# Optimization experiments

Hardware: AMD Instinct MI355X
Metric: run time of the kernel (lower is better)

## Reference

```python
import jax, jax.numpy as jnp
import numpy as np
import math

N_HEADS = 16
DIM = 1024
D_HEAD = DIM // N_HEADS
BS, QLEN = 2, 2048


def setup_inputs() -> dict:
    key = jax.random.key(0)
    ks = jax.random.split(key, 10)
    s = 0.02
    return {
        "input": jax.random.normal(ks[0], (BS, QLEN, DIM), dtype=jnp.float32),
        "mask": jnp.ones((BS, QLEN), dtype=jnp.int32),
        "q_w": jax.random.normal(ks[1], (DIM, DIM), dtype=jnp.float32) * s,
        "q_b": jax.random.normal(ks[2], (DIM,), dtype=jnp.float32) * s,
        "k_w": jax.random.normal(ks[3], (DIM, DIM), dtype=jnp.float32) * s,
        "k_b": jax.random.normal(ks[4], (DIM,), dtype=jnp.float32) * s,
        "v_w": jax.random.normal(ks[5], (DIM, DIM), dtype=jnp.float32) * s,
        "v_b": jax.random.normal(ks[6], (DIM,), dtype=jnp.float32) * s,
        "o_w": jax.random.normal(ks[7], (DIM, DIM), dtype=jnp.float32) * s,
        "o_b": jax.random.normal(ks[8], (DIM,), dtype=jnp.float32) * s,
    }


def _shape(x, bs):
    # (bs, len, dim) -> (bs, heads, len, d_head)
    return x.reshape(bs, -1, N_HEADS, D_HEAD).transpose(0, 2, 1, 3)


def reference(input, mask, q_w, q_b, k_w, k_b, v_w, v_b, o_w, o_b):
    bs, qlen, dim = input.shape
    # projections (torch Linear: x @ W^T + b)
    q = _shape(input @ q_w.T + q_b, bs)
    k = _shape(input @ k_w.T + k_b, bs)
    v = _shape(input @ v_w.T + v_b, bs)
    q = q / math.sqrt(D_HEAD)
    # scores: (bs, heads, qlen, klen)
    scores = jnp.einsum("bhqd,bhkd->bhqk", q, k)
    pad = (mask == 0)[:, None, None, :]  # (bs,1,1,klen)
    scores = jnp.where(pad, -jnp.inf, scores)
    weights = jax.nn.softmax(scores.astype(jnp.float32), axis=-1).astype(scores.dtype)
    # dropout p=0.0 (eval) -> identity
    context = jnp.einsum("bhqk,bhkd->bhqd", weights, v)
    context = context.transpose(0, 2, 1, 3).reshape(bs, qlen, dim)
    return context @ o_w.T + o_b
```

## Files before the change

### kernel.cpp

```cpp
#include <hip/hip_runtime.h>


#define BS    2
#define QLEN  2048
#define DIM   1024
#define NH    16
#define DH    64
#define MTOK  (BS * QLEN)

#define QSCALE 0.18033688011112042f

typedef __attribute__((ext_vector_type(8))) short short8;
typedef __attribute__((ext_vector_type(4))) float float4_t;
typedef __attribute__((ext_vector_type(4))) int   int4_t;

__device__ __forceinline__ ushort f2bf(float f) {
    unsigned u = __float_as_uint(f);
    return (ushort)((u + 0x7fffu + ((u >> 16) & 1u)) >> 16);
}
__device__ __forceinline__ short8 pack8(float4 a0, float4 a1) {
    short8 r;
    r[0] = (short)f2bf(a0.x); r[1] = (short)f2bf(a0.y);
    r[2] = (short)f2bf(a0.z); r[3] = (short)f2bf(a0.w);
    r[4] = (short)f2bf(a1.x); r[5] = (short)f2bf(a1.y);
    r[6] = (short)f2bf(a1.z); r[7] = (short)f2bf(a1.w);
    return r;
}

__device__ __forceinline__ void glds16(const void* g, void* l) {
    __builtin_amdgcn_global_load_lds(
        (const __attribute__((address_space(1))) unsigned int*)g,
        (__attribute__((address_space(3))) unsigned int*)l, 16, 0, 0);
}

__global__ __launch_bounds__(256) void conv_all(
    const float* __restrict__ x,  const float* __restrict__ qw,
    const float* __restrict__ kw, const float* __restrict__ vw,
    const float* __restrict__ ow,
    ushort* __restrict__ Xbf, ushort* __restrict__ Wbf)
{
    const int blk = blockIdx.x;
    const float* s; ushort* d; size_t base;
    if (blk < 4096)      { s = x;  d = Xbf;             base = (size_t)blk * 1024; }
    else if (blk < 5120) { s = qw; d = Wbf;             base = (size_t)(blk - 4096) * 1024; }
    else if (blk < 6144) { s = kw; d = Wbf + 1048576;   base = (size_t)(blk - 5120) * 1024; }
    else if (blk < 7168) { s = vw; d = Wbf + 2097152;   base = (size_t)(blk - 6144) * 1024; }
    else                 { s = ow; d = Wbf + 3145728;   base = (size_t)(blk - 7168) * 1024; }
    const size_t i = base + threadIdx.x * 4;
    float4 v = *(const float4*)(s + i);
    ushort4 o;
    o.x = f2bf(v.x); o.y = f2bf(v.y); o.z = f2bf(v.z); o.w = f2bf(v.w);
    *(ushort4*)(d + i) = o;
}

__global__ __launch_bounds__(256) void transpose_v(
    const ushort* __restrict__ Vrow, ushort* __restrict__ Vt)
{
    __shared__ ushort T[64][72];
    const int tid  = threadIdx.x;
    const int tile = blockIdx.x;
    const int bh   = blockIdx.y;
    const int b = bh >> 4, h = bh & 15;

    #pragma unroll
    for (int rep = 0; rep < 2; ++rep) {
        int ch = tid + rep * 256;
        int tok = ch >> 3, seg = ch & 7;
        uint4 v = *(const uint4*)(Vrow + (size_t)(b * QLEN + tile * 64 + tok) * DIM
                                        + h * DH + seg * 8);
        *(uint4*)&T[tok][seg * 8] = v;
    }
    __syncthreads();
    #pragma unroll
    for (int rep = 0; rep < 2; ++rep) {
        int ch = tid + rep * 256;
        int dim = ch >> 3, tseg = ch & 7;
        ushort t0 = T[tseg * 8 + 0][dim], t1 = T[tseg * 8 + 1][dim];
        ushort t2 = T[tseg * 8 + 2][dim], t3 = T[tseg * 8 + 3][dim];
        ushort t4 = T[tseg * 8 + 4][dim], t5 = T[tseg * 8 + 5][dim];
        ushort t6 = T[tseg * 8 + 6][dim], t7 = T[tseg * 8 + 7][dim];
        uint4 o;
        o.x = (unsigned)t0 | ((unsigned)t1 << 16);
        o.y = (unsigned)t2 | ((unsigned)t3 << 16);
        o.z = (unsigned)t4 | ((unsigned)t5 << 16);
        o.w = (unsigned)t6 | ((unsigned)t7 << 16);
        *(uint4*)(Vt + (size_t)bh * DH * QLEN + (size_t)dim * QLEN
                      + tile * 64 + tseg * 8) = o;
    }
}

__global__ __launch_bounds__(512, 2) void gemm_qkv(
    const ushort* __restrict__ A, const ushort* __restrict__ Bw,
    const float* __restrict__ bias0, const float* __restrict__ bias1,
    const float* __restrict__ bias2,
    ushort* __restrict__ outQ, ushort* __restrict__ outK, ushort* __restrict__ outVt)
{
    __shared__ ushort As[2][256 * 64];
    __shared__ ushort Bs[2][192 * 64];

    const int tid  = threadIdx.x;
    const int w    = tid >> 6;
    const int lane = tid & 63;
    const int r15  = lane & 15;
    const int quad = lane >> 4;
    const int wm   = w >> 2;
    const int wn   = w & 3;
    const int xg   = r15 & 7;

    const int xcd = blockIdx.x & 7;
    const int lid = blockIdx.x >> 3;
    const int brow = (xcd & 3) * 4 + (lid & 3);
    const int bcol = (xcd >> 2) * 8 + (lid >> 2);
    const int K = DIM;

    float4_t acc[8][3];
    #pragma unroll
    for (int i = 0; i < 8; ++i)
        #pragma unroll
        for (int j = 0; j < 3; ++j)
            acc[i][j] = (float4_t){0.f, 0.f, 0.f, 0.f};

    const ushort* gaS[4];
    const ushort* gbS[3];
    #pragma unroll
    for (int rep = 0; rep < 4; ++rep) {
        const int c   = rep * 512 + tid;
        const int row = c >> 3;
        const int g   = (c & 7) ^ (row & 7);
        gaS[rep] = A + (size_t)(brow * 256 + row) * K + g * 8;
    }
    #pragma unroll
    for (int rep = 0; rep < 3; ++rep) {
        const int c   = rep * 512 + tid;
        const int row = c >> 3;
        const int g   = (c & 7) ^ (row & 7);
        gbS[rep] = Bw + (size_t)(bcol * 192 + row) * K + g * 8;
    }

    short8 afr[2][4];
    short8 bfr[2][3];

#define QBAR() do { asm volatile("" ::: "memory");                            \
                    __builtin_amdgcn_s_barrier();                             \
                    asm volatile("" ::: "memory"); } while (0)
#define QVM0() asm volatile("s_waitcnt vmcnt(0)" ::: "memory")

#define STAGE_T(BUFI, KOFF) do {                                              \
    _Pragma("unroll")                                                         \
    for (int rep = 0; rep < 4; ++rep)                                         \
        glds16(gaS[rep] + (KOFF), &As[BUFI][(rep * 512 + tid) * 8]);          \
    _Pragma("unroll")                                                         \
    for (int rep = 0; rep < 3; ++rep)                                         \
        glds16(gbS[rep] + (KOFF), &Bs[BUFI][(rep * 512 + tid) * 8]);          \
} while (0)

#define PH_B(BUFI) do {                                                       \
    _Pragma("unroll")                                                         \
    for (int hh = 0; hh < 2; ++hh) {                                          \
        const int ph = ((hh * 4 + quad) ^ xg) * 8;                            \
        _Pragma("unroll")                                                     \
        for (int ns = 0; ns < 3; ++ns)                                        \
            bfr[hh][ns] = *(const short8*)&Bs[BUFI][(wn * 48 + ns * 16 + r15) * 64 + ph]; \
    }                                                                         \
} while (0)

#define PH_A(BUFI, MH) do {                                                   \
    const int arow0 = wm * 128 + (MH) * 64;                                   \
    _Pragma("unroll")                                                         \
    for (int hh = 0; hh < 2; ++hh) {                                          \
        const int ph = ((hh * 4 + quad) ^ xg) * 8;                            \
        _Pragma("unroll")                                                     \
        for (int ms = 0; ms < 4; ++ms)                                        \
            afr[hh][ms] = *(const short8*)&As[BUFI][(arow0 + ms * 16 + r15) * 64 + ph]; \
    }                                                                         \
} while (0)

#define MFMA_MH(MH) do {                                                      \
    __builtin_amdgcn_s_setprio(1);                                            \
    _Pragma("unroll")                                                         \
    for (int hh = 0; hh < 2; ++hh)                                            \
        _Pragma("unroll")                                                     \
        for (int ms = 0; ms < 4; ++ms)                                        \
            _Pragma("unroll")                                                 \
            for (int ns = 0; ns < 3; ++ns)                                    \
                acc[(MH) * 4 + ms][ns] =                                      \
                    __builtin_amdgcn_mfma_f32_16x16x32_bf16(                  \
                        afr[hh][ms], bfr[hh][ns], acc[(MH) * 4 + ms][ns], 0, 0, 0); \
    __builtin_amdgcn_s_setprio(0);                                            \
} while (0)

#define QITER(KB, LAST) do {                                                  \
    STAGE_T(1, (KB) + 64);                                                    \
    PH_B(0); PH_A(0, 0); MFMA_MH(0);                 QBAR();                  \
    PH_A(0, 1); MFMA_MH(1); QVM0();                  QBAR();                  \
    if (!(LAST)) STAGE_T(0, (KB) + 128);                                      \
    PH_B(1); PH_A(1, 0); MFMA_MH(0);                 QBAR();                  \
    PH_A(1, 1); MFMA_MH(1); if (!(LAST)) { QVM0(); } QBAR();                  \
} while (0)

    STAGE_T(0, 0);
    QVM0();
    QBAR();

    for (int i = 0; i < 7; ++i)
        QITER(i * 128, 0);
    QITER(896, 1);

#undef QITER
#undef MFMA_MH
#undef PH_A
#undef PH_B
#undef STAGE_T
#undef QVM0
#undef QBAR

    #pragma unroll
    for (int msg = 0; msg < 8; ++msg) {
        const int rowg = brow * 256 + wm * 128 + msg * 16 + quad * 4;
        #pragma unroll
        for (int nsg = 0; nsg < 3; ++nsg) {
            const int colg = bcol * 192 + wn * 48 + nsg * 16 + r15;
            if (colg < 1024) {
                const float bb = bias0[colg];
                #pragma unroll
                for (int r = 0; r < 4; ++r)
                    outQ[(size_t)(rowg + r) * 1024 + colg] =
                        f2bf((acc[msg][nsg][r] + bb) * QSCALE);
            } else if (colg < 2048) {
                const float bb = bias1[colg - 1024];
                #pragma unroll
                for (int r = 0; r < 4; ++r)
                    outK[(size_t)(rowg + r) * 1024 + (colg - 1024)] =
                        f2bf(acc[msg][nsg][r] + bb);
            } else {
                const int vcol = colg - 2048;
                const int hh2 = vcol >> 6, dd = vcol & 63;
                const float bb = bias2[vcol];
                const int bidx = rowg >> 11;
                const int tloc = rowg & 2047;
                ushort4 o4;
                o4.x = f2bf(acc[msg][nsg][0] + bb);
                o4.y = f2bf(acc[msg][nsg][1] + bb);
                o4.z = f2bf(acc[msg][nsg][2] + bb);
                o4.w = f2bf(acc[msg][nsg][3] + bb);
                *(ushort4*)&outVt[((size_t)(bidx * 16 + hh2) * 64 + dd) * QLEN + tloc] = o4;
            }
        }
    }
}

__global__ __launch_bounds__(256) void gemm_o(
    const ushort* __restrict__ A, const ushort* __restrict__ Bw,
    const float* __restrict__ bias, float* __restrict__ Out)
{
    __shared__ ushort As[2][128 * 64];
    __shared__ ushort Bs[2][64 * 64];
    const int tid  = threadIdx.x;
    const int w    = tid >> 6;
    const int lane = tid & 63;
    const int r15  = lane & 15;
    const int quad = lane >> 4;
    const int xcd = blockIdx.x & 7;
    const int lid = blockIdx.x >> 3;
    const int brow = (xcd & 3) * 8 + (lid & 7);
    const int bcol = (xcd >> 2) * 8 + (lid >> 3);
    const int wrow = w * 32;
    const int K = DIM;

    float4_t acc[2][4];
    #pragma unroll
    for (int i = 0; i < 2; ++i)
        #pragma unroll
        for (int j = 0; j < 4; ++j)
            acc[i][j] = (float4_t){0.f, 0.f, 0.f, 0.f};

    int chA[4];  const ushort* gaS[4];
    #pragma unroll
    for (int rep = 0; rep < 4; ++rep) {
        const int ch  = w * 256 + rep * 64 + lane;
        const int row = ch >> 3;
        const int g   = (ch & 7) ^ (row & 7);
        chA[rep] = ch;
        gaS[rep] = A + (size_t)(brow * 128 + row) * K + g * 8;
    }
    int chB[2];  const ushort* gbS[2];
    #pragma unroll
    for (int rep = 0; rep < 2; ++rep) {
        const int ch  = w * 128 + rep * 64 + lane;
        const int row = ch >> 3;
        const int g   = (ch & 7) ^ (row & 7);
        chB[rep] = ch;
        gbS[rep] = Bw + (size_t)(bcol * 64 + row) * K + g * 8;
    }
    const int xg = r15 & 7;

    #pragma unroll
    for (int rep = 0; rep < 4; ++rep)
        glds16(gaS[rep], &As[0][chA[rep] * 8]);
    #pragma unroll
    for (int rep = 0; rep < 2; ++rep)
        glds16(gbS[rep], &Bs[0][chB[rep] * 8]);
    __syncthreads();

    int p = 0;
    for (int k0 = 0; k0 < K; k0 += 64) {
        if (k0 + 64 < K) {
            #pragma unroll
            for (int rep = 0; rep < 4; ++rep)
                glds16(gaS[rep] + k0 + 64, &As[p ^ 1][chA[rep] * 8]);
            #pragma unroll
            for (int rep = 0; rep < 2; ++rep)
                glds16(gbS[rep] + k0 + 64, &Bs[p ^ 1][chB[rep] * 8]);
        }
        #pragma unroll
        for (int hh = 0; hh < 2; ++hh) {
            const int ph = ((hh * 4 + quad) ^ xg) * 8;
            short8 af[2], bf[4];
            #pragma unroll
            for (int ms = 0; ms < 2; ++ms)
                af[ms] = *(const short8*)&As[p][(wrow + ms * 16 + r15) * 64 + ph];
            #pragma unroll
            for (int ns = 0; ns < 4; ++ns)
                bf[ns] = *(const short8*)&Bs[p][(ns * 16 + r15) * 64 + ph];
            #pragma unroll
            for (int ms = 0; ms < 2; ++ms)
                #pragma unroll
                for (int ns = 0; ns < 4; ++ns)
                    acc[ms][ns] = __builtin_amdgcn_mfma_f32_16x16x32_bf16(
                        af[ms], bf[ns], acc[ms][ns], 0, 0, 0);
        }
        __syncthreads();
        p ^= 1;
    }

    #pragma unroll
    for (int ms = 0; ms < 2; ++ms) {
        const int rowg = brow * 128 + wrow + ms * 16 + quad * 4;
        #pragma unroll
        for (int ns = 0; ns < 4; ++ns) {
            const int colg = bcol * 64 + ns * 16 + r15;
            const float bb = bias[colg];
            #pragma unroll
            for (int r = 0; r < 4; ++r)
                Out[(size_t)(rowg + r) * 1024 + colg] = acc[ms][ns][r] + bb;
        }
    }
}

__global__ __launch_bounds__(256) void gemm_f32in_bf16out(
    const float* __restrict__ X, const float* __restrict__ W,
    const float* __restrict__ B, ushort* __restrict__ Out,
    int M, int N, int K, float scale)
{
    const int lane = threadIdx.x & 63;
    const int wid  = (blockIdx.x * blockDim.x + threadIdx.x) >> 6;
    const int tilesN = N >> 4;
    const int tm = wid / tilesN;
    const int tn = wid - tm * tilesN;
    const int r15  = lane & 15;
    const int quad = lane >> 4;

    const float* xp = X + (size_t)(tm * 16 + r15) * K + quad * 8;
    const float* wp = W + (size_t)(tn * 16 + r15) * K + quad * 8;

    float4_t acc = {0.f, 0.f, 0.f, 0.f};
    for (int k0 = 0; k0 < K; k0 += 32) {
        float4 a0 = *(const float4*)(xp + k0);
        float4 a1 = *(const float4*)(xp + k0 + 4);
        float4 b0 = *(const float4*)(wp + k0);
        float4 b1 = *(const float4*)(wp + k0 + 4);
        acc = __builtin_amdgcn_mfma_f32_16x16x32_bf16(pack8(a0, a1), pack8(b0, b1), acc, 0, 0, 0);
    }
    const int col  = tn * 16 + r15;
    const float bias = B[col];
    const int row0 = tm * 16 + quad * 4;
    #pragma unroll
    for (int r = 0; r < 4; ++r)
        Out[(size_t)(row0 + r) * N + col] = f2bf((acc[r] + bias) * scale);
}

__global__ __launch_bounds__(256) void gemm_bf16in_f32out(
    const ushort* __restrict__ X, const float* __restrict__ W,
    const float* __restrict__ B, float* __restrict__ Out,
    int M, int N, int K)
{
    const int lane = threadIdx.x & 63;
    const int wid  = (blockIdx.x * blockDim.x + threadIdx.x) >> 6;
    const int tilesN = N >> 4;
    const int tm = wid / tilesN;
    const int tn = wid - tm * tilesN;
    const int r15  = lane & 15;
    const int quad = lane >> 4;

    const ushort* xp = X + (size_t)(tm * 16 + r15) * K + quad * 8;
    const float*  wp = W + (size_t)(tn * 16 + r15) * K + quad * 8;

    float4_t acc = {0.f, 0.f, 0.f, 0.f};
    for (int k0 = 0; k0 < K; k0 += 32) {
        short8 a = *(const short8*)(xp + k0);
        float4 b0 = *(const float4*)(wp + k0);
        float4 b1 = *(const float4*)(wp + k0 + 4);
        acc = __builtin_amdgcn_mfma_f32_16x16x32_bf16(a, pack8(b0, b1), acc, 0, 0, 0);
    }
    const int col  = tn * 16 + r15;
    const float bias = B[col];
    const int row0 = tm * 16 + quad * 4;
    #pragma unroll
    for (int r = 0; r < 4; ++r)
        Out[(size_t)(row0 + r) * N + col] = acc[r] + bias;
}

__global__ __launch_bounds__(256, 2) void flash_attn(
    const ushort* __restrict__ Qb, const ushort* __restrict__ Kb,
    const ushort* __restrict__ Vt, const int* __restrict__ mask,
    ushort* __restrict__ Cb)
{
    __shared__ __align__(16) ushort Ks[2][64][64];
    __shared__ __align__(16) ushort Vs[4][64][64];
    __shared__ __align__(16) float  Mb[QLEN];

    const int tid  = threadIdx.x;
    const int w    = tid >> 6;
    const int lane = tid & 63;
    const int r15  = lane & 15;
    const int quad = lane >> 4;
    const int flat = blockIdx.x;
    const int xcd  = flat & 7;
    const int j    = flat >> 3;
    const int bh   = xcd + 8 * (j >> 4);
    const int qt   = j & 15;
    const int b = bh >> 4, h = bh & 15;

    {
        const int4* m4 = (const int4*)(mask + b * QLEN);
        #pragma unroll
        for (int rep = 0; rep < 2; ++rep) {
            const int idx = tid + rep * 256;
            int4 mv = m4[idx];
            float4 o;
            o.x = mv.x ? 0.f : -INFINITY;
            o.y = mv.y ? 0.f : -INFINITY;
            o.z = mv.z ? 0.f : -INFINITY;
            o.w = mv.w ? 0.f : -INFINITY;
            *(float4*)&Mb[idx * 4] = o;
        }
    }

    const int qbase = qt * 128 + w * 32;
    const ushort* qp = Qb + (size_t)(b * QLEN + qbase + r15) * DIM + h * DH + quad * 8;
    short8 qf[2][2];
    qf[0][0] = *(const short8*)(qp);
    qf[0][1] = *(const short8*)(qp + 32);
    qf[1][0] = *(const short8*)(qp + 16 * DIM);
    qf[1][1] = *(const short8*)(qp + 16 * DIM + 32);

    const ushort* kg = Kb + (size_t)b * QLEN * DIM + h * DH;
    const ushort* vg = Vt + (size_t)bh * DH * QLEN;

    const int a0 = tid >> 3, seg = tid & 7;
    const int krow0 = (((a0 & 7) >> 2) << 4) + (((a0 >> 3) & 3) << 2) + (a0 & 3);
    const int sK = (seg ^ (krow0 & 7)) << 3;
    const int sV = (seg ^ (a0 & 7)) << 3;
    const int xq = (quad ^ (r15 & 7)) << 3;

    float4_t o[2][4];
    float4_t ol[2];
    #pragma unroll
    for (int rg = 0; rg < 2; ++rg) {
        ol[rg] = (float4_t){0.f, 0.f, 0.f, 0.f};
        #pragma unroll
        for (int ds = 0; ds < 4; ++ds)
            o[rg][ds] = (float4_t){0.f, 0.f, 0.f, 0.f};
    }
    short8 ones8;
    #pragma unroll
    for (int i = 0; i < 8; ++i) ones8[i] = (short)0x3F80;

    uint4 kr0, kr1, vr0, vr1;
    int pkA[4][2][2], pkB[4][2][2];

#define LOAD_TILE(KT) do {                                                    \
    kr0 = *(const uint4*)(kg + (size_t)((KT) + a0     ) * DIM  + seg * 8);    \
    kr1 = *(const uint4*)(kg + (size_t)((KT) + a0 + 32) * DIM  + seg * 8);    \
    vr0 = *(const uint4*)(vg + (size_t)(a0     ) * QLEN + (KT) + seg * 8);    \
    vr1 = *(const uint4*)(vg + (size_t)(a0 + 32) * QLEN + (KT) + seg * 8);    \
} while (0)

#define STORE_TILE(KBUF, VBUF) do {                                           \
    *(uint4*)&Ks[KBUF][krow0     ][sK] = kr0;                                 \
    *(uint4*)&Ks[KBUF][krow0 + 32][sK] = kr1;                                 \
    *(uint4*)&Vs[VBUF][a0        ][sV] = vr0;                                 \
    *(uint4*)&Vs[VBUF][a0 + 32   ][sV] = vr1;                                 \
} while (0)

#define S_PHASE(KBUF, KT, PK) do {                                            \
    _Pragma("unroll")                                                         \
    for (int ks = 0; ks < 4; ++ks) {                                          \
        const ushort* krow = &Ks[KBUF][ks * 16 + r15][0];                     \
        short8 kf0 = *(const short8*)(krow + xq);                             \
        short8 kf1 = *(const short8*)(krow + (xq ^ 32));                      \
        const float4 mb = *(const float4*)&Mb[(KT) + ((ks >> 1) << 5)         \
                                              + (quad << 3) + ((ks & 1) << 2)]; \
        _Pragma("unroll")                                                     \
        for (int rg = 0; rg < 2; ++rg) {                                      \
            float4_t s = {0.f, 0.f, 0.f, 0.f};                                \
            s = __builtin_amdgcn_mfma_f32_16x16x32_bf16(kf0, qf[rg][0], s, 0, 0, 0); \
            s = __builtin_amdgcn_mfma_f32_16x16x32_bf16(kf1, qf[rg][1], s, 0, 0, 0); \
            unsigned u0 = __float_as_uint(__builtin_amdgcn_exp2f(s[0] + mb.x)); \
            unsigned u1 = __float_as_uint(__builtin_amdgcn_exp2f(s[1] + mb.y)); \
            unsigned u2 = __float_as_uint(__builtin_amdgcn_exp2f(s[2] + mb.z)); \
            unsigned u3 = __float_as_uint(__builtin_amdgcn_exp2f(s[3] + mb.w)); \
            PK[ks][rg][0] = __builtin_amdgcn_perm(u1, u0, 0x07060302);        \
            PK[ks][rg][1] = __builtin_amdgcn_perm(u3, u2, 0x07060302);        \
        }                                                                     \
    }                                                                         \
} while (0)

#define PV_PHASE(VBUF, PK) do {                                               \
    _Pragma("unroll")                                                         \
    for (int ck = 0; ck < 2; ++ck) {                                          \
        short8 vf[4];                                                         \
        _Pragma("unroll")                                                     \
        for (int ds = 0; ds < 4; ++ds)                                        \
            vf[ds] = *(const short8*)(&Vs[VBUF][ds * 16 + r15][0] + (xq ^ (ck << 5))); \
        _Pragma("unroll")                                                     \
        for (int rg = 0; rg < 2; ++rg) {                                      \
            int4_t pfi = { PK[2 * ck][rg][0], PK[2 * ck][rg][1],              \
                           PK[2 * ck + 1][rg][0], PK[2 * ck + 1][rg][1] };    \
            short8 pf = __builtin_bit_cast(short8, pfi);                      \
            _Pragma("unroll")                                                 \
            for (int ds = 0; ds < 4; ++ds)                                    \
                o[rg][ds] = __builtin_amdgcn_mfma_f32_16x16x32_bf16(          \
                    pf, vf[ds], o[rg][ds], 0, 0, 0);                          \
            ol[rg] = __builtin_amdgcn_mfma_f32_16x16x32_bf16(                 \
                pf, ones8, ol[rg], 0, 0, 0);                                  \
        }                                                                     \
    }                                                                         \
} while (0)

    LOAD_TILE(0);
    STORE_TILE(0, 0);
    LOAD_TILE(64);
    __syncthreads();
    S_PHASE(0, 0, pkA);
    STORE_TILE(1, 1);
    __syncthreads();
    LOAD_TILE(128);

    for (int kb = 0; kb < 1792; kb += 256) {
        S_PHASE(1, kb + 64, pkB);  PV_PHASE(0, pkA);
        STORE_TILE(0, 2); __syncthreads(); LOAD_TILE(kb + 192);
        S_PHASE(0, kb + 128, pkA); PV_PHASE(1, pkB);
        STORE_TILE(1, 3); __syncthreads(); LOAD_TILE(kb + 256);
        S_PHASE(1, kb + 192, pkB); PV_PHASE(2, pkA);
        STORE_TILE(0, 0); __syncthreads(); LOAD_TILE(kb + 320);
        S_PHASE(0, kb + 256, pkA); PV_PHASE(3, pkB);
        STORE_TILE(1, 1); __syncthreads(); LOAD_TILE(kb + 384);
    }

    S_PHASE(1, 1856, pkB); PV_PHASE(0, pkA);
    STORE_TILE(0, 2); __syncthreads(); LOAD_TILE(1984);
    S_PHASE(0, 1920, pkA); PV_PHASE(1, pkB);
    STORE_TILE(1, 3); __syncthreads();
    S_PHASE(1, 1984, pkB); PV_PHASE(2, pkA);
    PV_PHASE(3, pkB);

#undef LOAD_TILE
#undef STORE_TILE
#undef S_PHASE
#undef PV_PHASE

    #pragma unroll
    for (int rg = 0; rg < 2; ++rg) {
        #pragma unroll
        for (int r = 0; r < 4; ++r) {
            const float ir = 1.f / fmaxf(ol[rg][r], 1e-30f);
            const size_t rb = (size_t)(b * QLEN + qbase + rg * 16 + quad * 4 + r) * DIM
                              + h * DH;
            Cb[rb +  0 + r15] = f2bf(o[rg][0][r] * ir);
            Cb[rb + 16 + r15] = f2bf(o[rg][1][r] * ir);
            Cb[rb + 32 + r15] = f2bf(o[rg][2][r] * ir);
            Cb[rb + 48 + r15] = f2bf(o[rg][3][r] * ir);
        }
    }
}

extern "C" void kernel_launch(void* const* d_in, const int* in_sizes, int n_in,
                              void* d_out, int out_size, void* d_ws, size_t ws_size,
                              hipStream_t stream)
{
    const float* x    = (const float*)d_in[0];
    const int*   mask = (const int*)d_in[1];
    const float* q_w  = (const float*)d_in[2];
    const float* q_b  = (const float*)d_in[3];
    const float* k_w  = (const float*)d_in[4];
    const float* k_b  = (const float*)d_in[5];
    const float* v_w  = (const float*)d_in[6];
    const float* v_b  = (const float*)d_in[7];
    const float* o_w  = (const float*)d_in[8];
    const float* o_b  = (const float*)d_in[9];
    float* out = (float*)d_out;

    const size_t SEG = (size_t)MTOK * DIM;
    ushort* Qbf = (ushort*)d_out;
    ushort* Xbf = Qbf + SEG;
    ushort* Kb  = (ushort*)d_ws;
    ushort* Cb  = Kb + SEG;
    ushort* Vt  = Cb + SEG;
    ushort* Wbf = Vt + SEG;

    const bool big = ws_size >= (size_t)32 * 1024 * 1024;

    if (big) {
        conv_all<<<8192, 256, 0, stream>>>(x, q_w, k_w, v_w, o_w, Xbf, Wbf);
        gemm_qkv<<<(MTOK / 256) * (3072 / 192), 512, 0, stream>>>(
            Xbf, Wbf, q_b, k_b, v_b, Qbf, Kb, Vt);
        flash_attn<<<(QLEN / 128) * (BS * NH), 256, 0, stream>>>(Qbf, Kb, Vt, mask, Cb);
        gemm_o<<<(MTOK / 128) * (DIM / 64), 256, 0, stream>>>(
            Cb, Wbf + 3 * (size_t)(DIM * DIM), o_b, out);
    } else {
        const int tiles   = (MTOK / 16) * (DIM / 16);
        const int gblocks = tiles / 4;
        gemm_f32in_bf16out<<<gblocks, 256, 0, stream>>>(x, q_w, q_b, Qbf, MTOK, DIM, DIM, QSCALE);
        gemm_f32in_bf16out<<<gblocks, 256, 0, stream>>>(x, k_w, k_b, Kb,  MTOK, DIM, DIM, 1.0f);
        gemm_f32in_bf16out<<<gblocks, 256, 0, stream>>>(x, v_w, v_b, Cb,  MTOK, DIM, DIM, 1.0f);
        transpose_v<<<dim3(QLEN / 64, BS * NH), 256, 0, stream>>>(Cb, Vt);
        flash_attn<<<(QLEN / 128) * (BS * NH), 256, 0, stream>>>(Qbf, Kb, Vt, mask, Cb);
        gemm_bf16in_f32out<<<tiles / 4, 256, 0, stream>>>(Cb, o_w, o_b, out, MTOK, DIM, DIM);
    }
}
```

Before: 186.9 us.

## Enlarge flash-attention and output-GEMM blocks to 512 threads with deeper pipelining

```diff
diff --git a/kernel.cpp b/kernel.cpp
--- a/kernel.cpp
+++ b/kernel.cpp
@@ -249,100 +249,135 @@
     }
 }
 
-__global__ __launch_bounds__(256) void gemm_o(
+__global__ __launch_bounds__(512, 2) void gemm_o(
     const ushort* __restrict__ A, const ushort* __restrict__ Bw,
     const float* __restrict__ bias, float* __restrict__ Out)
 {
-    __shared__ ushort As[2][128 * 64];
+    __shared__ ushort As[2][256 * 64];
     __shared__ ushort Bs[2][64 * 64];
+
     const int tid  = threadIdx.x;
     const int w    = tid >> 6;
     const int lane = tid & 63;
     const int r15  = lane & 15;
     const int quad = lane >> 4;
+    const int wm   = w >> 1;
+    const int wn   = w & 1;
+    const int xg   = r15 & 7;
+
     const int xcd = blockIdx.x & 7;
     const int lid = blockIdx.x >> 3;
-    const int brow = (xcd & 3) * 8 + (lid & 7);
-    const int bcol = (xcd >> 2) * 8 + (lid >> 3);
-    const int wrow = w * 32;
+    const int brow = (xcd & 3) * 4 + (lid & 3);
+    const int bcol = (xcd >> 2) * 8 + (lid >> 2);
     const int K = DIM;
 
-    float4_t acc[2][4];
-    #pragma unroll
-    for (int i = 0; i < 2; ++i)
+    float4_t acc[4][2];
+    #pragma unroll
+    for (int i = 0; i < 4; ++i)
         #pragma unroll
-        for (int j = 0; j < 4; ++j)
+        for (int j = 0; j < 2; ++j)
             acc[i][j] = (float4_t){0.f, 0.f, 0.f, 0.f};
 
-    int chA[4];  const ushort* gaS[4];
+    const ushort* gaS[4];
     #pragma unroll
     for (int rep = 0; rep < 4; ++rep) {
-        const int ch  = w * 256 + rep * 64 + lane;
-        const int row = ch >> 3;
-        const int g   = (ch & 7) ^ (row & 7);
-        chA[rep] = ch;
-        gaS[rep] = A + (size_t)(brow * 128 + row) * K + g * 8;
-    }
-    int chB[2];  const ushort* gbS[2];
-    #pragma unroll
-    for (int rep = 0; rep < 2; ++rep) {
-        const int ch  = w * 128 + rep * 64 + lane;
-        const int row = ch >> 3;
-        const int g   = (ch & 7) ^ (row & 7);
-        chB[rep] = ch;
-        gbS[rep] = Bw + (size_t)(bcol * 64 + row) * K + g * 8;
-    }
-    const int xg = r15 & 7;
-
-    #pragma unroll
-    for (int rep = 0; rep < 4; ++rep)
-        glds16(gaS[rep], &As[0][chA[rep] * 8]);
-    #pragma unroll
-    for (int rep = 0; rep < 2; ++rep)
-        glds16(gbS[rep], &Bs[0][chB[rep] * 8]);
-    __syncthreads();
-
-    int p = 0;
-    for (int k0 = 0; k0 < K; k0 += 64) {
-        if (k0 + 64 < K) {
-            #pragma unroll
-            for (int rep = 0; rep < 4; ++rep)
-                glds16(gaS[rep] + k0 + 64, &As[p ^ 1][chA[rep] * 8]);
-            #pragma unroll
-            for (int rep = 0; rep < 2; ++rep)
-                glds16(gbS[rep] + k0 + 64, &Bs[p ^ 1][chB[rep] * 8]);
-        }
+        const int c   = rep * 512 + tid;
+        const int row = c >> 3;
+        const int g   = (c & 7) ^ (row & 7);
+        gaS[rep] = A + (size_t)(brow * 256 + row) * K + g * 8;
+    }
+    const ushort* gbS;
+    {
+        const int row = tid >> 3;
+        const int g   = (tid & 7) ^ (row & 7);
+        gbS = Bw + (size_t)(bcol * 64 + row) * K + g * 8;
+    }
+
+    short8 afr[2][2];
+    short8 bfr[2][2];
+
+#define OBAR() do { asm volatile("" ::: "memory");                            \
+                    __builtin_amdgcn_s_barrier();                             \
+                    asm volatile("" ::: "memory"); } while (0)
+#define OVM0() asm volatile("s_waitcnt vmcnt(0)" ::: "memory")
+
+#define OSTAGE(BUFI, KOFF) do {                                               \
+    _Pragma("unroll")                                                         \
+    for (int rep = 0; rep < 4; ++rep)                                         \
+        glds16(gaS[rep] + (KOFF), &As[BUFI][(rep * 512 + tid) * 8]);          \
+    glds16(gbS + (KOFF), &Bs[BUFI][tid * 8]);                                 \
+} while (0)
+
+#define OPH_B(BUFI) do {                                                      \
+    _Pragma("unroll")                                                         \
+    for (int hh = 0; hh < 2; ++hh) {                                          \
+        const int ph = ((hh * 4 + quad) ^ xg) * 8;                            \
+        _Pragma("unroll")                                                     \
+        for (int ns = 0; ns < 2; ++ns)                                        \
+            bfr[hh][ns] = *(const short8*)&Bs[BUFI][(wn * 32 + ns * 16 + r15) * 64 + ph]; \
+    }                                                                         \
+} while (0)
+
+#define OPH_A(BUFI, MH) do {                                                  \
+    const int arow0 = wm * 64 + (MH) * 32;                                    \
+    _Pragma("unroll")                                                         \
+    for (int hh = 0; hh < 2; ++hh) {                                          \
+        const int ph = ((hh * 4 + quad) ^ xg) * 8;                            \
+        _Pragma("unroll")                                                     \
+        for (int ms = 0; ms < 2; ++ms)                                        \
+            afr[hh][ms] = *(const short8*)&As[BUFI][(arow0 + ms * 16 + r15) * 64 + ph]; \
+    }                                                                         \
+} while (0)
+
+#define OMFMA(MH) do {                                                        \
+    __builtin_amdgcn_s_setprio(1);                                            \
+    _Pragma("unroll")                                                         \
+    for (int hh = 0; hh < 2; ++hh)                                            \
+        _Pragma("unroll")                                                     \
+        for (int ms = 0; ms < 2; ++ms)                                        \
+            _Pragma("unroll")                                                 \
+            for (int ns = 0; ns < 2; ++ns)                                    \
+                acc[(MH) * 2 + ms][ns] =                                      \
+                    __builtin_amdgcn_mfma_f32_16x16x32_bf16(                  \
+                        afr[hh][ms], bfr[hh][ns], acc[(MH) * 2 + ms][ns], 0, 0, 0); \
+    __builtin_amdgcn_s_setprio(0);                                            \
+} while (0)
+
+#define OITER(KB, LAST) do {                                                  \
+    OSTAGE(1, (KB) + 64);                                                     \
+    OPH_B(0); OPH_A(0, 0); OMFMA(0);                 OBAR();                  \
+    OPH_A(0, 1); OMFMA(1); OVM0();                   OBAR();                  \
+    if (!(LAST)) OSTAGE(0, (KB) + 128);                                       \
+    OPH_B(1); OPH_A(1, 0); OMFMA(0);                 OBAR();                  \
+    OPH_A(1, 1); OMFMA(1); if (!(LAST)) { OVM0(); }  OBAR();                  \
+} while (0)
+
+    OSTAGE(0, 0);
+    OVM0();
+    OBAR();
+
+    for (int i = 0; i < 7; ++i)
+        OITER(i * 128, 0);
+    OITER(896, 1);
+
+#undef OITER
+#undef OMFMA
+#undef OPH_A
+#undef OPH_B
+#undef OSTAGE
+#undef OVM0
+#undef OBAR
+
+    #pragma unroll
+    for (int msg = 0; msg < 4; ++msg) {
+        const int rowg = brow * 256 + wm * 64 + msg * 16 + quad * 4;
         #pragma unroll
-        for (int hh = 0; hh < 2; ++hh) {
-            const int ph = ((hh * 4 + quad) ^ xg) * 8;
-            short8 af[2], bf[4];
-            #pragma unroll
-            for (int ms = 0; ms < 2; ++ms)
-                af[ms] = *(const short8*)&As[p][(wrow + ms * 16 + r15) * 64 + ph];
-            #pragma unroll
-            for (int ns = 0; ns < 4; ++ns)
-                bf[ns] = *(const short8*)&Bs[p][(ns * 16 + r15) * 64 + ph];
-            #pragma unroll
-            for (int ms = 0; ms < 2; ++ms)
-                #pragma unroll
-                for (int ns = 0; ns < 4; ++ns)
-                    acc[ms][ns] = __builtin_amdgcn_mfma_f32_16x16x32_bf16(
-                        af[ms], bf[ns], acc[ms][ns], 0, 0, 0);
-        }
-        __syncthreads();
-        p ^= 1;
-    }
-
-    #pragma unroll
-    for (int ms = 0; ms < 2; ++ms) {
-        const int rowg = brow * 128 + wrow + ms * 16 + quad * 4;
-        #pragma unroll
-        for (int ns = 0; ns < 4; ++ns) {
-            const int colg = bcol * 64 + ns * 16 + r15;
+        for (int nsg = 0; nsg < 2; ++nsg) {
+            const int colg = bcol * 64 + wn * 32 + nsg * 16 + r15;
             const float bb = bias[colg];
             #pragma unroll
             for (int r = 0; r < 4; ++r)
-                Out[(size_t)(rowg + r) * 1024 + colg] = acc[ms][ns][r] + bb;
+                Out[(size_t)(rowg + r) * 1024 + colg] = acc[msg][nsg][r] + bb;
         }
     }
 }
@@ -410,7 +445,7 @@
         Out[(size_t)(row0 + r) * N + col] = acc[r] + bias;
 }
 
-__global__ __launch_bounds__(256, 2) void flash_attn(
+__global__ __launch_bounds__(512, 2) void flash_attn(
     const ushort* __restrict__ Qb, const ushort* __restrict__ Kb,
     const ushort* __restrict__ Vt, const int* __restrict__ mask,
     ushort* __restrict__ Cb)
@@ -427,26 +462,22 @@
     const int flat = blockIdx.x;
     const int xcd  = flat & 7;
     const int j    = flat >> 3;
-    const int bh   = xcd + 8 * (j >> 4);
-    const int qt   = j & 15;
+    const int bh   = xcd + 8 * (j >> 3);
+    const int qt   = j & 7;
     const int b = bh >> 4, h = bh & 15;
 
     {
         const int4* m4 = (const int4*)(mask + b * QLEN);
-        #pragma unroll
-        for (int rep = 0; rep < 2; ++rep) {
-            const int idx = tid + rep * 256;
-            int4 mv = m4[idx];
-            float4 o;
-            o.x = mv.x ? 0.f : -INFINITY;
-            o.y = mv.y ? 0.f : -INFINITY;
-            o.z = mv.z ? 0.f : -INFINITY;
-            o.w = mv.w ? 0.f : -INFINITY;
-            *(float4*)&Mb[idx * 4] = o;
-        }
-    }
-
-    const int qbase = qt * 128 + w * 32;
+        int4 mv = m4[tid];
+        float4 o;
+        o.x = mv.x ? 0.f : -INFINITY;
+        o.y = mv.y ? 0.f : -INFINITY;
+        o.z = mv.z ? 0.f : -INFINITY;
+        o.w = mv.w ? 0.f : -INFINITY;
+        *(float4*)&Mb[tid * 4] = o;
+    }
+
+    const int qbase = qt * 256 + w * 32;
     const ushort* qp = Qb + (size_t)(b * QLEN + qbase + r15) * DIM + h * DH + quad * 8;
     short8 qf[2][2];
     qf[0][0] = *(const short8*)(qp);
@@ -458,7 +489,9 @@
     const ushort* vg = Vt + (size_t)bh * DH * QLEN;
 
     const int a0 = tid >> 3, seg = tid & 7;
-    const int krow0 = (((a0 & 7) >> 2) << 4) + (((a0 >> 3) & 3) << 2) + (a0 & 3);
+    const int a5 = a0 & 31;
+    const int krow0 = (a0 & 32)
+                    | ((((a5 & 7) >> 2) << 4) + (((a5 >> 3) & 3) << 2) + (a5 & 3));
     const int sK = (seg ^ (krow0 & 7)) << 3;
     const int sV = (seg ^ (a0 & 7)) << 3;
     const int xq = (quad ^ (r15 & 7)) << 3;
@@ -476,21 +509,17 @@
     #pragma unroll
     for (int i = 0; i < 8; ++i) ones8[i] = (short)0x3F80;
 
-    uint4 kr0, kr1, vr0, vr1;
+    uint4 kr0, vr0;
     int pkA[4][2][2], pkB[4][2][2];
 
 #define LOAD_TILE(KT) do {                                                    \
-    kr0 = *(const uint4*)(kg + (size_t)((KT) + a0     ) * DIM  + seg * 8);    \
-    kr1 = *(const uint4*)(kg + (size_t)((KT) + a0 + 32) * DIM  + seg * 8);    \
-    vr0 = *(const uint4*)(vg + (size_t)(a0     ) * QLEN + (KT) + seg * 8);    \
-    vr1 = *(const uint4*)(vg + (size_t)(a0 + 32) * QLEN + (KT) + seg * 8);    \
+    kr0 = *(const uint4*)(kg + (size_t)((KT) + a0) * DIM  + seg * 8);         \
+    vr0 = *(const uint4*)(vg + (size_t)a0 * QLEN + (KT) + seg * 8);           \
 } while (0)
 
 #define STORE_TILE(KBUF, VBUF) do {                                           \
-    *(uint4*)&Ks[KBUF][krow0     ][sK] = kr0;                                 \
-    *(uint4*)&Ks[KBUF][krow0 + 32][sK] = kr1;                                 \
-    *(uint4*)&Vs[VBUF][a0        ][sV] = vr0;                                 \
-    *(uint4*)&Vs[VBUF][a0 + 32   ][sV] = vr1;                                 \
+    *(uint4*)&Ks[KBUF][krow0][sK] = kr0;                                      \
+    *(uint4*)&Vs[VBUF][a0   ][sV] = vr0;                                      \
 } while (0)
 
 #define S_PHASE(KBUF, KT, PK) do {                                            \
@@ -615,8 +644,8 @@
         conv_all<<<8192, 256, 0, stream>>>(x, q_w, k_w, v_w, o_w, Xbf, Wbf);
         gemm_qkv<<<(MTOK / 256) * (3072 / 192), 512, 0, stream>>>(
             Xbf, Wbf, q_b, k_b, v_b, Qbf, Kb, Vt);
-        flash_attn<<<(QLEN / 128) * (BS * NH), 256, 0, stream>>>(Qbf, Kb, Vt, mask, Cb);
-        gemm_o<<<(MTOK / 128) * (DIM / 64), 256, 0, stream>>>(
+        flash_attn<<<(QLEN / 256) * (BS * NH), 512, 0, stream>>>(Qbf, Kb, Vt, mask, Cb);
+        gemm_o<<<(MTOK / 256) * (DIM / 64), 512, 0, stream>>>(
             Cb, Wbf + 3 * (size_t)(DIM * DIM), o_b, out);
     } else {
         const int tiles   = (MTOK / 16) * (DIM / 16);
@@ -625,7 +654,7 @@
         gemm_f32in_bf16out<<<gblocks, 256, 0, stream>>>(x, k_w, k_b, Kb,  MTOK, DIM, DIM, 1.0f);
         gemm_f32in_bf16out<<<gblocks, 256, 0, stream>>>(x, v_w, v_b, Cb,  MTOK, DIM, DIM, 1.0f);
         transpose_v<<<dim3(QLEN / 64, BS * NH), 256, 0, stream>>>(Cb, Vt);
-        flash_attn<<<(QLEN / 128) * (BS * NH), 256, 0, stream>>>(Qbf, Kb, Vt, mask, Cb);
+        flash_attn<<<(QLEN / 256) * (BS * NH), 512, 0, stream>>>(Qbf, Kb, Vt, mask, Cb);
         gemm_bf16in_f32out<<<tiles / 4, 256, 0, stream>>>(Cb, o_w, o_b, out, MTOK, DIM, DIM);
     }
 }
```

After: 187.2 us. About the same (+0.2%).
